# Performance work log

Hardware: AMD Instinct MI355X
Metric: run time of the kernel (lower is better)

The kernel has to match this reference:

```python
import jax, jax.numpy as jnp
import numpy as np

TARGET_MAIN_CONTRIBUTION = 0.6
CONTRIB_LOSS_COEF = 0.01
TOP_K = 2
NEG_INF = -1e9


def _gat(x, adj, W1, a1s, a1d, W2, a2s, a2d):
    """Dense 2-layer GAT (pyGAT style): multi-head concat + ELU, then one output head.
    x: [B,S,Fin], adj: [B,S,S], W1: [H,Fin,Fh], a1s/a1d: [H,Fh], W2: [H*Fh,Fout], a2s/a2d: [Fout]."""
    mask = adj > 0  # [B,S,S]
    h = jnp.einsum('bsf,hfo->bhso', x, W1)                      # [B,H,S,Fh]
    es = jnp.einsum('bhso,ho->bhs', h, a1s)
    ed = jnp.einsum('bhso,ho->bhs', h, a1d)
    e = jax.nn.leaky_relu(es[:, :, :, None] + ed[:, :, None, :], 0.2)  # [B,H,S,S]
    att = jax.nn.softmax(jnp.where(mask[:, None], e, NEG_INF), axis=-1)
    h1 = jax.nn.elu(jnp.einsum('bhst,bhto->bhso', att, h))      # [B,H,S,Fh]
    B, H, S, Fh = h1.shape
    h1 = h1.transpose(0, 2, 1, 3).reshape(B, S, H * Fh)         # concat heads
    h2 = h1 @ W2                                                # [B,S,Fout]
    e2 = jax.nn.leaky_relu((h2 @ a2s)[:, :, None] + (h2 @ a2d)[:, None, :], 0.2)
    att2 = jax.nn.softmax(jnp.where(mask, e2, NEG_INF), axis=-1)
    return jnp.einsum('bst,bto->bso', att2, h2)


def setup_inputs() -> dict:
    B, S, D, H, Hd, E = 4, 1024, 256, 6, 64, 3
    key = jax.random.key(0)
    ks = jax.random.split(key, 20)
    feature = jax.random.normal(ks[0], (B, S, D), dtype=jnp.float32)
    # sparse-ish binary adjacency with self-loops
    adj = (jax.random.uniform(ks[1], (B, S, S)) < 0.05).astype(jnp.float32)
    adj = jnp.maximum(adj, jnp.eye(S, dtype=jnp.float32)[None])
    p = lambda k, shape: jax.random.normal(k, shape, dtype=jnp.float32) * 0.1
    return {
        'feature': feature, 'adj': adj,
        'main_W1': p(ks[2], (H, D, Hd)), 'main_a1s': p(ks[3], (H, Hd)), 'main_a1d': p(ks[4], (H, Hd)),
        'main_W2': p(ks[5], (H * Hd, D)), 'main_a2s': p(ks[6], (D,)), 'main_a2d': p(ks[7], (D,)),
        'dep_W1': p(ks[8], (E, H, D, Hd)), 'dep_a1s': p(ks[9], (E, H, Hd)), 'dep_a1d': p(ks[10], (E, H, Hd)),
        'dep_W2': p(ks[11], (E, H * Hd, D)), 'dep_a2s': p(ks[12], (E, D)), 'dep_a2d': p(ks[13], (E, D)),
        'router_W': p(ks[14], (D, E)),
        'blend_W': p(ks[15], (D, D)), 'blend_b': jnp.zeros((D,), dtype=jnp.float32),
        'doc_num': 4, 'sect_num': 32,
    }


def reference(feature, adj, main_W1, main_a1s, main_a1d, main_W2, main_a2s, main_a2d,
              dep_W1, dep_a1s, dep_a1d, dep_W2, dep_a2s, dep_a2d,
              router_W, blend_W, blend_b, doc_num, sect_num):
    B, S, D = feature.shape
    E = router_W.shape[1]
    # main expert on full graph
    main_output = _gat(feature, adj, main_W1, main_a1s, main_a1d, main_W2, main_a2s, main_a2d)
    # per-expert adjacency views (zero out columns by node type)
    col = jnp.arange(S)
    sent_cols = (col < S - sect_num - doc_num).astype(adj.dtype)
    sect_cols = ((col >= S - sect_num - doc_num) & (col < S - doc_num)).astype(adj.dtype)
    doc_cols = (col >= S - doc_num).astype(adj.dtype)
    adj_stack = jnp.stack([adj * sent_cols, adj * sect_cols, adj * doc_cols])  # [E,B,S,S]
    # fixed top-k router
    x_flat = feature.reshape(-1, D)
    gate_probs = jax.nn.softmax(x_flat @ router_W, axis=-1)      # [B*S,E]
    _, top_idx = jax.lax.top_k(gate_probs, TOP_K)                # [B*S,k]
    routing_mask = jax.nn.one_hot(top_idx, E, dtype=feature.dtype).sum(axis=-2)  # [B*S,E] binary
    routing_mask = routing_mask.reshape(B, S, E)
    mask_e = routing_mask.transpose(2, 0, 1)[..., None]          # [E,B,S,1]
    # deputy experts: masked input, masked output, accumulate
    x_e = feature[None] * mask_e                                 # [E,B,S,D]
    dep_out = jax.vmap(_gat)(x_e, adj_stack, dep_W1, dep_a1s, dep_a1d, dep_W2, dep_a2s, dep_a2d)
    deputy_output = (dep_out * mask_e).sum(axis=0)               # [B,S,D]
    # blend gate
    blend_weight = jax.nn.sigmoid(feature @ blend_W + blend_b)
    final_output = blend_weight * main_output + (1.0 - blend_weight) * deputy_output
    main_contribution = blend_weight.mean()
    contribution_loss = jnp.abs(main_contribution - TARGET_MAIN_CONTRIBUTION) * CONTRIB_LOSS_COEF
    return final_output, contribution_loss, main_contribution
```

## Files before the change

kernel.cpp:

```cpp
#include <hip/hip_runtime.h>
#include <math.h>

#define B 4
#define S 1024
#define D 256
#define H 6
#define HD 64
#define NE 3
#define HHD 384
#define ROWS (B*S)
#define MAXN 128

typedef __attribute__((ext_vector_type(8))) short bf8_t;
typedef __attribute__((ext_vector_type(4))) float f32x4;

__device__ __forceinline__ float leaky(float x){ return x > 0.f ? x : 0.2f*x; }

__device__ __forceinline__ unsigned short f2bf(float f){
    union { float f; unsigned int u; } v; v.f = f;
    unsigned int u = v.u;
    return (unsigned short)((u + 0x7FFFu + ((u >> 16) & 1u)) >> 16);
}
__device__ __forceinline__ float bf2f(unsigned short h){
    union { unsigned int u; float f; } v; v.u = ((unsigned int)h) << 16;
    return v.f;
}
__device__ __forceinline__ float blo(unsigned int u){
    union { unsigned int u; float f; } v; v.u = u << 16; return v.f;
}
__device__ __forceinline__ float bhi(unsigned int u){
    union { unsigned int u; float f; } v; v.u = u & 0xffff0000u; return v.f;
}
__device__ __forceinline__ float i2f(int t){
    union { int i; float f; } v; v.i = t; return v.f;
}
__device__ __forceinline__ int f2i(float f){
    union { float f; int i; } v; v.f = f; return v.i;
}

#define PB_CONV   1024
#define PB_NBR    1024
#define PB_W1     1536
#define PB_W2     1536
#define PB_BW      256
#define PB_ZERO    177
#define PB_ROUTER 1024
#define PB_TOTAL  (PB_CONV + PB_NBR + PB_W1 + PB_W2 + PB_BW + PB_ZERO + PB_ROUTER)
#define NZERO     45088

__global__ __launch_bounds__(256) void prep_misc_kernel(
        const float* __restrict__ feature, const float* __restrict__ adj,
        const float* __restrict__ main_W1, const float* __restrict__ dep_W1,
        const float* __restrict__ main_W2, const float* __restrict__ dep_W2,
        const float* __restrict__ blend_W, const float* __restrict__ router_W,
        const int* __restrict__ doc_p, const int* __restrict__ sect_p,
        unsigned short* __restrict__ featbf, short* __restrict__ nbr,
        int4* __restrict__ nbc, unsigned short* __restrict__ w1nk,
        unsigned short* __restrict__ w2nk, unsigned short* __restrict__ bwt,
        float* __restrict__ zbase, float* __restrict__ rmask)
{
    int blk = blockIdx.x, tid = threadIdx.x;
    if (blk < PB_CONV){
        int idx = blk*256 + tid;
        float4 v = ((const float4*)feature)[idx];
        ushort4 o;
        o.x = f2bf(v.x); o.y = f2bf(v.y); o.z = f2bf(v.z); o.w = f2bf(v.w);
        ((ushort4*)featbf)[idx] = o;
        return;
    }
    blk -= PB_CONV;
    if (blk < PB_NBR){
        int wave = tid >> 6, lane = tid & 63;
        int row = blk*4 + wave;
        int b1 = S - *sect_p - *doc_p;
        int b2 = S - *doc_p;
        const float* ar = adj + (size_t)row*S + lane*16;
        float a[16];
        #pragma unroll
        for (int q = 0; q < 4; q++){
            float4 v = ((const float4*)ar)[q];
            a[q*4+0] = v.x; a[q*4+1] = v.y; a[q*4+2] = v.z; a[q*4+3] = v.w;
        }
        int t0 = lane*16;
        int k = 0, c1 = 0, c2 = 0;
        #pragma unroll
        for (int i = 0; i < 16; i++){
            if (a[i] > 0.f){
                k++;
                int t = t0 + i;
                if (t < b1) c1++;
                if (t < b2) c2++;
            }
        }
        int inc = k;
        #pragma unroll
        for (int d = 1; d < 64; d <<= 1){
            int u = __shfl_up(inc, d);
            if (lane >= d) inc += u;
        }
        int off = inc - k;
        int total = __shfl(inc, 63);
        int o = row*MAXN + off;
        #pragma unroll
        for (int i = 0; i < 16; i++){
            if (a[i] > 0.f) nbr[o++] = (short)(t0 + i);
        }
        for (int d = 32; d; d >>= 1){
            c1 += __shfl_down(c1, d);
            c2 += __shfl_down(c2, d);
        }
        if (lane == 0) nbc[row] = make_int4(total, c1, c2, 0);
        return;
    }
    blk -= PB_NBR;
    if (blk < PB_W1){
        int e = blk / 384;
        int idx = (blk - e*384)*256 + tid;
        const float* src = (e == 0) ? main_W1 : dep_W1 + (size_t)(e-1)*H*D*HD;
        int n = idx >> 8, k = idx & 255;
        int h = n >> 6, o = n & 63;
        w1nk[(size_t)e*HHD*D + idx] = f2bf(src[(h*D + k)*HD + o]);
        return;
    }
    blk -= PB_W1;
    if (blk < PB_W2){
        int g = blk*256 + tid;
        int e = g / (D*HHD);
        int rem = g - e*(D*HHD);
        int n = rem / HHD, k = rem - n*HHD;
        const float* src = (e == 0) ? main_W2 : dep_W2 + (size_t)(e-1)*HHD*D;
        w2nk[g] = f2bf(src[k*D + n]);
        return;
    }
    blk -= PB_W2;
    if (blk < PB_BW){
        int col = blk, k = tid;
        bwt[col*D + k] = f2bf(blend_W[k*D + col]);
        return;
    }
    blk -= PB_BW;
    if (blk < PB_ZERO){
        int idx = blk*256 + tid;
        if (idx < NZERO) zbase[idx] = 0.f;
        return;
    }
    blk -= PB_ZERO;
    {
        int wave = tid >> 6, lane = tid & 63;
        int row = blk*4 + wave;
        float4 xv = ((const float4*)(feature + (size_t)row*D))[lane];
        int f = lane*4;
        float xa[4] = {xv.x, xv.y, xv.z, xv.w};
        float p0 = 0.f, p1 = 0.f, p2 = 0.f;
        #pragma unroll
        for (int j = 0; j < 4; j++){
            p0 += xa[j]*router_W[(f+j)*NE + 0];
            p1 += xa[j]*router_W[(f+j)*NE + 1];
            p2 += xa[j]*router_W[(f+j)*NE + 2];
        }
        for (int off = 32; off; off >>= 1){
            p0 += __shfl_down(p0, off);
            p1 += __shfl_down(p1, off);
            p2 += __shfl_down(p2, off);
        }
        if (lane == 0){
            float p[3] = {p0, p1, p2};
            int ex = 0;
            for (int e = 1; e < NE; e++) if (p[e] <= p[ex]) ex = e;
            for (int e = 0; e < NE; e++) rmask[e*ROWS + row] = (e == ex) ? 0.f : 1.f;
        }
    }
}

__global__ __launch_bounds__(256) void gemm1_kernel(const unsigned short* __restrict__ w1nk,
                                                    const unsigned short* __restrict__ featbf,
                                                    const float* __restrict__ rmask,
                                                    const float* __restrict__ main_a1s,
                                                    const float* __restrict__ main_a1d,
                                                    const float* __restrict__ dep_a1s,
                                                    const float* __restrict__ dep_a1d,
                                                    unsigned short* __restrict__ htn4,
                                                    float* __restrict__ es8,
                                                    float* __restrict__ ed8,
                                                    float* __restrict__ meanV1p){
    __shared__ float ep[2][64][17];
    int tid = threadIdx.x, wave = tid >> 6, lane = tid & 63;
    int quad = lane >> 4, l16 = lane & 15;
    int e = blockIdx.z;
    int m0 = blockIdx.x*64;
    int n0 = blockIdx.y*64;
    const unsigned short* arow = w1nk + (size_t)e*HHD*D + (size_t)(m0 + wave*16 + l16)*D + quad*8;
    const unsigned short* brow[4];
    bool zr[4];
    #pragma unroll
    for (int j = 0; j < 4; j++){
        int n = n0 + j*16 + l16;
        brow[j] = featbf + (size_t)n*D + quad*8;
        zr[j] = (e > 0) ? (rmask[(size_t)(e-1)*ROWS + n] == 0.f) : false;
    }
    f32x4 z4 = {0.f,0.f,0.f,0.f};
    f32x4 acc[4] = {z4, z4, z4, z4};
    bf8_t bz = {0,0,0,0,0,0,0,0};
    for (int k0 = 0; k0 < D; k0 += 32){
        bf8_t a = *(const bf8_t*)(arow + k0);
        #pragma unroll
        for (int j = 0; j < 4; j++){
            bf8_t bv = zr[j] ? bz : *(const bf8_t*)(brow[j] + k0);
            acc[j] = __builtin_amdgcn_mfma_f32_16x16x32_bf16(a, bv, acc[j], 0, 0, 0);
        }
    }
    int b = n0 >> 10;
    int mbase = m0 + wave*16 + quad*4;
    int obase = wave*16 + quad*4;
    #pragma unroll
    for (int j = 0; j < 4; j++){
        int row = n0 + j*16 + l16;
        ushort4 o;
        o.x = f2bf(acc[j][0]); o.y = f2bf(acc[j][1]);
        o.z = f2bf(acc[j][2]); o.w = f2bf(acc[j][3]);
        *(ushort4*)(htn4 + ((size_t)e*ROWS + row)*HHD + mbase) = o;
    }
    const float* a1sp = (e == 0) ? main_a1s : dep_a1s + (size_t)(e-1)*H*HD;
    const float* a1dp = (e == 0) ? main_a1d : dep_a1d + (size_t)(e-1)*H*HD;
    float a1sv[4], a1dv[4];
    #pragma unroll
    for (int r = 0; r < 4; r++){ a1sv[r] = a1sp[mbase + r]; a1dv[r] = a1dp[mbase + r]; }
    #pragma unroll
    for (int j = 0; j < 4; j++){
        float ps = 0.f, pd = 0.f;
        #pragma unroll
        for (int r = 0; r < 4; r++){ ps += acc[j][r]*a1sv[r]; pd += acc[j][r]*a1dv[r]; }
        ep[0][j*16 + l16][wave*4 + quad] = ps;
        ep[1][j*16 + l16][wave*4 + quad] = pd;
    }
    #pragma unroll
    for (int r = 0; r < 4; r++){
        float cm = acc[0][r] + acc[1][r] + acc[2][r] + acc[3][r];
        for (int off = 8; off; off >>= 1) cm += __shfl_down(cm, off, 16);
        if (l16 == 0)
            atomicAdd(meanV1p + ((size_t)e*B + b)*512 + (obase + r)*8 + blockIdx.x,
                      cm*(1.f/(float)S));
    }
    __syncthreads();
    if (tid < 128){
        int arr = tid >> 6, sl = tid & 63;
        float sum = 0.f;
        #pragma unroll
        for (int i = 0; i < 16; i++) sum += ep[arr][sl][i];
        int n = n0 + sl;
        float* dst = arr ? ed8 : es8;
        dst[(((size_t)e*B + (n >> 10))*S + (n & 1023))*8 + blockIdx.x] = sum;
    }
}

__global__ __launch_bounds__(256) void remap1_kernel(const unsigned short* __restrict__ htn4,
                                                     unsigned short* __restrict__ V1p,
                                                     const int* __restrict__ doc_p,
                                                     const int* __restrict__ sect_p){
    int t = blockIdx.x, b = blockIdx.y, e = blockIdx.z;
    int b1 = S - *sect_p - *doc_p;
    int b2 = S - *doc_p;
    if (e == 1 && t >= b1) return;
    if (e == 2 && (t < b1 || t >= b2)) return;
    if (e == 3 && t < b2) return;
    if (e >= 2 && t < 960) return;
    unsigned short* dst;
    if (e < 2) dst = V1p + ((size_t)(e*B + b)*S + t)*512;
    else       dst = V1p + ((size_t)(2*B)*S + ((size_t)((e-2)*B + b))*64 + (t - 960))*512;
    const unsigned short* src = htn4 + ((size_t)e*ROWS + b*S + t)*HHD;
    int tid = threadIdx.x;
    int c0 = tid*2;
    int o = c0 >> 3, h = c0 & 7;
    unsigned short v0 = (h < 6)   ? src[h*64 + o]       : (unsigned short)0;
    unsigned short v1 = (h+1 < 6) ? src[(h+1)*64 + o]   : (unsigned short)0;
    ushort2 ov; ov.x = v0; ov.y = v1;
    *(ushort2*)(dst + c0) = ov;
}

__global__ __launch_bounds__(256) void attn1_gather_kernel(const unsigned short* __restrict__ V1p,
                                                           const float* __restrict__ es8,
                                                           const float* __restrict__ ed8,
                                                           const short* __restrict__ nbr,
                                                           const int4* __restrict__ nbc,
                                                           const float* __restrict__ meanV1p,
                                                           unsigned short* __restrict__ h1c4){
    __shared__ float wrec[4][MAXN][8];
    int wave = threadIdx.x >> 6, lane = threadIdx.x & 63;
    int s = blockIdx.x*4 + wave;
    int e = blockIdx.y >> 2, b = blockIdx.y & 3;
    int row = b*S + s;
    int4 c = nbc[row];
    int lo = 0, hi = c.x;
    if (e == 1) hi = c.y;
    else if (e == 2){ lo = c.y; hi = c.z; }
    else if (e == 3){ lo = c.z; }
    int nn = hi - lo;
    const float* esp = es8 + (((size_t)e*B + b)*S + s)*8;
    f32x4 es_lo = *(const f32x4*)esp;
    f32x4 es_hi = *(const f32x4*)(esp + 4);
    float esv[6] = {es_lo[0], es_lo[1], es_lo[2], es_lo[3], es_hi[0], es_hi[1]};
    const float* edb = ed8 + (((size_t)e*B + b)*S)*8;
    const short* nl = nbr + (size_t)row*MAXN;
    float w0[6] = {0,0,0,0,0,0}, w1[6] = {0,0,0,0,0,0};
    int t0 = 0, t1 = 0;
    if (lane < nn){
        t0 = nl[lo + lane];
        const float* ep = edb + (size_t)t0*8;
        f32x4 d0 = *(const f32x4*)ep;
        f32x4 d1 = *(const f32x4*)(ep + 4);
        float edv[6] = {d0[0], d0[1], d0[2], d0[3], d1[0], d1[1]};
        #pragma unroll
        for (int h = 0; h < 6; h++) w0[h] = __expf(leaky(esv[h] + edv[h]));
    }
    if (64 + lane < nn){
        t1 = nl[lo + 64 + lane];
        const float* ep = edb + (size_t)t1*8;
        f32x4 d0 = *(const f32x4*)ep;
        f32x4 d1 = *(const f32x4*)(ep + 4);
        float edv[6] = {d0[0], d0[1], d0[2], d0[3], d1[0], d1[1]};
        #pragma unroll
        for (int h = 0; h < 6; h++) w1[h] = __expf(leaky(esv[h] + edv[h]));
    }
    float den[6];
    #pragma unroll
    for (int h = 0; h < 6; h++){
        float d = w0[h] + w1[h];
        for (int o2 = 32; o2; o2 >>= 1) d += __shfl_down(d, o2);
        den[h] = __shfl(d, 0);
    }
    if (lane < nn){
        f32x4 r0 = {w0[0], w0[1], w0[2], w0[3]};
        f32x4 r1 = {w0[4], w0[5], i2f(t0), 0.f};
        *(f32x4*)&wrec[wave][lane][0] = r0;
        *(f32x4*)&wrec[wave][lane][4] = r1;
    }
    if (64 + lane < nn){
        f32x4 r0 = {w1[0], w1[1], w1[2], w1[3]};
        f32x4 r1 = {w1[4], w1[5], i2f(t1), 0.f};
        *(f32x4*)&wrec[wave][64 + lane][0] = r0;
        *(f32x4*)&wrec[wave][64 + lane][4] = r1;
    }
    const unsigned short* Vb;
    int toff;
    if (e < 2){ Vb = V1p + ((size_t)(e*B + b)*S)*512; toff = 0; }
    else      { Vb = V1p + ((size_t)(2*B)*S + ((size_t)((e-2)*B + b))*64)*512; toff = 960; }
    float acc[6] = {0,0,0,0,0,0};
    #pragma unroll 4
    for (int j = 0; j < nn; j++){
        f32x4 r0 = *(const f32x4*)&wrec[wave][j][0];
        f32x4 r1 = *(const f32x4*)&wrec[wave][j][4];
        int t = f2i(r1[2]);
        const unsigned short* vp = Vb + (size_t)(t - toff)*512 + lane*8;
        uint4 dv = *(const uint4*)vp;
        acc[0] += r0[0]*blo(dv.x); acc[1] += r0[1]*bhi(dv.x);
        acc[2] += r0[2]*blo(dv.y); acc[3] += r0[3]*bhi(dv.y);
        acc[4] += r1[0]*blo(dv.z); acc[5] += r1[1]*bhi(dv.z);
    }
    unsigned short* outp = h1c4 + ((size_t)e*ROWS + row)*HHD;
    const float* mv = meanV1p + ((size_t)e*B + b)*512 + lane*8;
    #pragma unroll
    for (int h = 0; h < 6; h++){
        float v = (nn > 0) ? acc[h]/den[h] : mv[h];
        v = v > 0.f ? v : __expf(v) - 1.f;
        outp[h*64 + lane] = f2bf(v);
    }
}

__global__ __launch_bounds__(256) void gemm2_kernel(const unsigned short* __restrict__ w2nk,
                                                    const unsigned short* __restrict__ h1c4,
                                                    const float* __restrict__ main_a2s,
                                                    const float* __restrict__ main_a2d,
                                                    const float* __restrict__ dep_a2s,
                                                    const float* __restrict__ dep_a2d,
                                                    unsigned short* __restrict__ h2n4,
                                                    float* __restrict__ f2s4,
                                                    float* __restrict__ f2d4,
                                                    float* __restrict__ meanV2){
    __shared__ float ep[2][64][17];
    int tid = threadIdx.x, wave = tid >> 6, lane = tid & 63;
    int quad = lane >> 4, l16 = lane & 15;
    int e = blockIdx.z;
    int m0 = blockIdx.x*64;
    int n0 = blockIdx.y*64;
    const unsigned short* arow = w2nk + (size_t)e*D*HHD + (size_t)(m0 + wave*16 + l16)*HHD + quad*8;
    const unsigned short* brow[4];
    #pragma unroll
    for (int j = 0; j < 4; j++)
        brow[j] = h1c4 + (size_t)e*ROWS*HHD + (size_t)(n0 + j*16 + l16)*HHD + quad*8;
    f32x4 z4 = {0.f,0.f,0.f,0.f};
    f32x4 acc[4] = {z4, z4, z4, z4};
    for (int k0 = 0; k0 < HHD; k0 += 32){
        bf8_t a = *(const bf8_t*)(arow + k0);
        #pragma unroll
        for (int j = 0; j < 4; j++){
            bf8_t bv = *(const bf8_t*)(brow[j] + k0);
            acc[j] = __builtin_amdgcn_mfma_f32_16x16x32_bf16(a, bv, acc[j], 0, 0, 0);
        }
    }
    int b = n0 >> 10;
    int mbase = m0 + wave*16 + quad*4;
    #pragma unroll
    for (int j = 0; j < 4; j++){
        int row = n0 + j*16 + l16;
        ushort4 o;
        o.x = f2bf(acc[j][0]); o.y = f2bf(acc[j][1]);
        o.z = f2bf(acc[j][2]); o.w = f2bf(acc[j][3]);
        *(ushort4*)(h2n4 + ((size_t)e*ROWS + row)*D + mbase) = o;
    }
    const float* a2sp = (e == 0) ? main_a2s : dep_a2s + (size_t)(e-1)*D;
    const float* a2dp = (e == 0) ? main_a2d : dep_a2d + (size_t)(e-1)*D;
    float a2sv[4], a2dv[4];
    #pragma unroll
    for (int r = 0; r < 4; r++){ a2sv[r] = a2sp[mbase + r]; a2dv[r] = a2dp[mbase + r]; }
    #pragma unroll
    for (int j = 0; j < 4; j++){
        float ps = 0.f, pd = 0.f;
        #pragma unroll
        for (int r = 0; r < 4; r++){ ps += acc[j][r]*a2sv[r]; pd += acc[j][r]*a2dv[r]; }
        ep[0][j*16 + l16][wave*4 + quad] = ps;
        ep[1][j*16 + l16][wave*4 + quad] = pd;
    }
    #pragma unroll
    for (int r = 0; r < 4; r++){
        float cm = acc[0][r] + acc[1][r] + acc[2][r] + acc[3][r];
        for (int off = 8; off; off >>= 1) cm += __shfl_down(cm, off, 16);
        if (l16 == 0)
            atomicAdd(meanV2 + ((size_t)e*B + b)*D + mbase + r, cm*(1.f/(float)S));
    }
    __syncthreads();
    if (tid < 128){
        int arr = tid >> 6, sl = tid & 63;
        float sum = 0.f;
        #pragma unroll
        for (int i = 0; i < 16; i++) sum += ep[arr][sl][i];
        int n = n0 + sl;
        float* dst = arr ? f2d4 : f2s4;
        atomicAdd(dst + (size_t)e*ROWS + n, sum);
    }
}

__global__ __launch_bounds__(256) void attn2_gather_kernel(const unsigned short* __restrict__ h2n4,
                                                           const float* __restrict__ f2s4,
                                                           const float* __restrict__ f2d4,
                                                           const short* __restrict__ nbr,
                                                           const int4* __restrict__ nbc,
                                                           const float* __restrict__ meanV2,
                                                           float* __restrict__ mainO,
                                                           unsigned short* __restrict__ depO3){
    __shared__ float2 wrec[4][MAXN];
    int wave = threadIdx.x >> 6, lane = threadIdx.x & 63;
    int s = blockIdx.x*4 + wave;
    int e = blockIdx.y >> 2, b = blockIdx.y & 3;
    int row = b*S + s;
    int4 c = nbc[row];
    int lo = 0, hi = c.x;
    if (e == 1) hi = c.y;
    else if (e == 2){ lo = c.y; hi = c.z; }
    else if (e == 3){ lo = c.z; }
    int nn = hi - lo;
    float fs_r = f2s4[(size_t)e*ROWS + row];
    const float* fdp = f2d4 + (size_t)e*ROWS + b*S;
    const short* nl = nbr + (size_t)row*MAXN;
    float w0 = 0.f, w1 = 0.f;
    int t0 = 0, t1 = 0;
    if (lane < nn){ t0 = nl[lo + lane]; w0 = __expf(leaky(fs_r + fdp[t0])); }
    if (64 + lane < nn){ t1 = nl[lo + 64 + lane]; w1 = __expf(leaky(fs_r + fdp[t1])); }
    float den = w0 + w1;
    for (int o2 = 32; o2; o2 >>= 1) den += __shfl_down(den, o2);
    den = __shfl(den, 0);
    if (lane < nn){ float2 r; r.x = w0; r.y = i2f(t0); wrec[wave][lane] = r; }
    if (64 + lane < nn){ float2 r; r.x = w1; r.y = i2f(t1); wrec[wave][64 + lane] = r; }
    const unsigned short* V = h2n4 + ((size_t)e*ROWS + b*S)*D;
    float acc[4] = {0,0,0,0};
    #pragma unroll 4
    for (int j = 0; j < nn; j++){
        float2 r = wrec[wave][j];
        float w = r.x;
        int t = f2i(r.y);
        const unsigned short* vp = V + (size_t)t*D + lane*4;
        uint2 dv = *(const uint2*)vp;
        acc[0] += w*blo(dv.x); acc[1] += w*bhi(dv.x);
        acc[2] += w*blo(dv.y); acc[3] += w*bhi(dv.y);
    }
    float out[4];
    if (nn > 0){
        float inv = 1.f/den;
        #pragma unroll
        for (int q = 0; q < 4; q++) out[q] = acc[q]*inv;
    } else {
        const float* mv = meanV2 + ((size_t)e*B + b)*D + lane*4;
        #pragma unroll
        for (int q = 0; q < 4; q++) out[q] = mv[q];
    }
    if (e == 0){
        *(float4*)(mainO + (size_t)row*D + lane*4) = make_float4(out[0], out[1], out[2], out[3]);
    } else {
        ushort4 o;
        o.x = f2bf(out[0]); o.y = f2bf(out[1]); o.z = f2bf(out[2]); o.w = f2bf(out[3]);
        *(ushort4*)(depO3 + (size_t)(e-1)*ROWS*D + (size_t)row*D + lane*4) = o;
    }
}

#define BLEND_NBLK ((ROWS/64)*(D/64))
__global__ __launch_bounds__(256) void blend_mfma_kernel(const unsigned short* __restrict__ featbf,
                                                         const unsigned short* __restrict__ bwt,
                                                         const float* __restrict__ bb,
                                                         const float* __restrict__ mainO,
                                                         const unsigned short* __restrict__ depO3,
                                                         const float* __restrict__ rmask,
                                                         float* __restrict__ outp,
                                                         float* __restrict__ sumBuf,
                                                         unsigned int* __restrict__ doneCnt){
    __shared__ float red[256];
    int tid = threadIdx.x, wave = tid >> 6, lane = tid & 63;
    int quad = lane >> 4, l16 = lane & 15;
    int m0 = blockIdx.x*64, n0 = blockIdx.y*64;
    const unsigned short* arow = featbf + (size_t)(m0 + wave*16 + l16)*D + quad*8;
    const unsigned short* brow[4];
    #pragma unroll
    for (int j = 0; j < 4; j++)
        brow[j] = bwt + (size_t)(n0 + j*16 + l16)*D + quad*8;
    f32x4 z4 = {0.f,0.f,0.f,0.f};
    f32x4 acc[4] = {z4, z4, z4, z4};
    for (int k0 = 0; k0 < D; k0 += 32){
        bf8_t a = *(const bf8_t*)(arow + k0);
        #pragma unroll
        for (int j = 0; j < 4; j++){
            bf8_t bv = *(const bf8_t*)(brow[j] + k0);
            acc[j] = __builtin_amdgcn_mfma_f32_16x16x32_bf16(a, bv, acc[j], 0, 0, 0);
        }
    }
    float lsum = 0.f;
    int mbase = m0 + wave*16 + quad*4;
    float rm[4][3];
    #pragma unroll
    for (int r = 0; r < 4; r++)
        #pragma unroll
        for (int e0 = 0; e0 < 3; e0++)
            rm[r][e0] = rmask[(size_t)e0*ROWS + mbase + r];
    #pragma unroll
    for (int j = 0; j < 4; j++){
        int col = n0 + j*16 + l16;
        float bias = bb[col];
        #pragma unroll
        for (int r = 0; r < 4; r++){
            size_t idx = (size_t)(mbase + r)*D + col;
            float dep = 0.f;
            #pragma unroll
            for (int e0 = 0; e0 < 3; e0++)
                dep += rm[r][e0]*bf2f(depO3[(size_t)e0*ROWS*D + idx]);
            float bw = 1.f/(1.f + __expf(-(acc[j][r] + bias)));
            lsum += bw;
            outp[idx] = bw*mainO[idx] + (1.f - bw)*dep;
        }
    }
    red[tid] = lsum;
    __syncthreads();
    for (int sft = 128; sft; sft >>= 1){
        if (tid < sft) red[tid] += red[tid + sft];
        __syncthreads();
    }
    if (tid == 0){
        atomicAdd(sumBuf, red[0]);
        __threadfence();
        unsigned int old = atomicAdd(doneCnt, 1u);
        if (old == BLEND_NBLK - 1){
            float total = atomicAdd(sumBuf, 0.f);
            float mc = total / (float)(ROWS*D);
            outp[ROWS*D]     = fabsf(mc - 0.6f)*0.01f;
            outp[ROWS*D + 1] = mc;
        }
    }
}

extern "C" void kernel_launch(void* const* d_in, const int* in_sizes, int n_in,
                              void* d_out, int out_size, void* d_ws, size_t ws_size,
                              hipStream_t stream)
{
    const float* feature  = (const float*)d_in[0];
    const float* adj      = (const float*)d_in[1];
    const float* main_W1  = (const float*)d_in[2];
    const float* main_a1s = (const float*)d_in[3];
    const float* main_a1d = (const float*)d_in[4];
    const float* main_W2  = (const float*)d_in[5];
    const float* main_a2s = (const float*)d_in[6];
    const float* main_a2d = (const float*)d_in[7];
    const float* dep_W1   = (const float*)d_in[8];
    const float* dep_a1s  = (const float*)d_in[9];
    const float* dep_a1d  = (const float*)d_in[10];
    const float* dep_W2   = (const float*)d_in[11];
    const float* dep_a2s  = (const float*)d_in[12];
    const float* dep_a2d  = (const float*)d_in[13];
    const float* router_W = (const float*)d_in[14];
    const float* blend_W  = (const float*)d_in[15];
    const float* blend_b  = (const float*)d_in[16];
    const int*   doc_p    = (const int*)d_in[17];
    const int*   sect_p   = (const int*)d_in[18];

    char* ws = (char*)d_ws;
    size_t off = 0;
    unsigned short* featbf = (unsigned short*)(ws + off); off += (size_t)ROWS*D*2;
    short*          nbr    = (short*)(ws + off);          off += (size_t)ROWS*MAXN*2;
    int4*           nbc    = (int4*)(ws + off);           off += (size_t)ROWS*16;
    unsigned short* w1nk   = (unsigned short*)(ws + off); off += (size_t)4*HHD*D*2;
    unsigned short* w2nk   = (unsigned short*)(ws + off); off += (size_t)4*D*HHD*2;
    unsigned short* bwt    = (unsigned short*)(ws + off); off += (size_t)D*D*2;
    float* es8 = (float*)(ws + off); off += (size_t)4*B*S*8*4;
    float* ed8 = (float*)(ws + off); off += (size_t)4*B*S*8*4;
    unsigned short* htn4 = (unsigned short*)(ws + off);
    float* mainO = (float*)(ws + off);
    unsigned short* depO3 = (unsigned short*)(ws + off + (size_t)ROWS*D*4);
    off += (size_t)4*ROWS*HHD*2;
    unsigned short* V1p  = (unsigned short*)(ws + off);
    unsigned short* h2n4 = (unsigned short*)(ws + off);
    {
        size_t v1sz = ((size_t)2*B*S + (size_t)2*B*64)*512*2;
        size_t h2sz = (size_t)4*ROWS*D*2;
        off += (v1sz > h2sz) ? v1sz : h2sz;
    }
    unsigned short* h1c4 = (unsigned short*)(ws + off); off += (size_t)4*ROWS*HHD*2;
    float* f2s4    = (float*)(ws + off); off += (size_t)4*ROWS*4;
    float* f2d4    = (float*)(ws + off); off += (size_t)4*ROWS*4;
    float* meanV1p = (float*)(ws + off); off += (size_t)4*B*512*4;
    float* meanV2  = (float*)(ws + off); off += (size_t)4*B*D*4;
    float* sumBuf  = (float*)(ws + off); off += 128;
    unsigned int* doneCnt = (unsigned int*)(sumBuf + 4);
    float* rmask   = (float*)(ws + off); off += (size_t)NE*ROWS*4;
    float* outp    = (float*)d_out;

    prep_misc_kernel<<<PB_TOTAL, 256, 0, stream>>>(
        feature, adj, main_W1, dep_W1, main_W2, dep_W2, blend_W, router_W,
        doc_p, sect_p, featbf, nbr, nbc, w1nk, w2nk, bwt, f2s4, rmask);

    gemm1_kernel<<<dim3(H, ROWS/64, 4), 256, 0, stream>>>(w1nk, featbf, rmask,
        main_a1s, main_a1d, dep_a1s, dep_a1d, htn4, es8, ed8, meanV1p);
    remap1_kernel<<<dim3(S, B, 4), 256, 0, stream>>>(htn4, V1p, doc_p, sect_p);
    attn1_gather_kernel<<<dim3(S/4, 16), 256, 0, stream>>>(V1p, es8, ed8, nbr, nbc,
        meanV1p, h1c4);
    gemm2_kernel<<<dim3(D/64, ROWS/64, 4), 256, 0, stream>>>(w2nk, h1c4,
        main_a2s, main_a2d, dep_a2s, dep_a2d, h2n4, f2s4, f2d4, meanV2);
    attn2_gather_kernel<<<dim3(S/4, 16), 256, 0, stream>>>(h2n4, f2s4, f2d4, nbr, nbc,
        meanV2, mainO, depO3);

    blend_mfma_kernel<<<dim3(ROWS/64, D/64), 256, 0, stream>>>(featbf, bwt, blend_b,
        mainO, depO3, rmask, outp, sumBuf, doneCnt);
}
```

Measured before the change: 243.3 us.

## Fuse V1 remap into gemm1 epilogue, retile blend kernel, deepen gather unroll

The gemm1 epilogue now writes its bf16 results straight into the head-interleaved V1p layout, with the expert-specific row-range filtering applied there. This removes the separate remap1 kernel along with the htn4 intermediate round trip through memory. The blend kernel is retiled to 16-row blocks with one MFMA tile per wave, giving four times as many blocks. The neighbour loops in both attention gathers are unrolled by 8 instead of 4. The cost is that the fused stores are strided 2-byte scatters, and the smaller blend blocks each reload their slice of bwt.

```diff
diff --git a/kernel.cpp b/kernel.cpp
--- a/kernel.cpp
+++ b/kernel.cpp
@@ -179,7 +179,9 @@
                                                     const float* __restrict__ main_a1d,
                                                     const float* __restrict__ dep_a1s,
                                                     const float* __restrict__ dep_a1d,
-                                                    unsigned short* __restrict__ htn4,
+                                                    const int* __restrict__ doc_p,
+                                                    const int* __restrict__ sect_p,
+                                                    unsigned short* __restrict__ V1p,
                                                     float* __restrict__ es8,
                                                     float* __restrict__ ed8,
                                                     float* __restrict__ meanV1p){
@@ -212,13 +214,34 @@
     int b = n0 >> 10;
     int mbase = m0 + wave*16 + quad*4;
     int obase = wave*16 + quad*4;
-    #pragma unroll
-    for (int j = 0; j < 4; j++){
-        int row = n0 + j*16 + l16;
-        ushort4 o;
-        o.x = f2bf(acc[j][0]); o.y = f2bf(acc[j][1]);
-        o.z = f2bf(acc[j][2]); o.w = f2bf(acc[j][3]);
-        *(ushort4*)(htn4 + ((size_t)e*ROWS + row)*HHD + mbase) = o;
+    int hh = blockIdx.x;
+    int b1v = S - *sect_p - *doc_p;
+    int b2v = S - *doc_p;
+    int tbase = n0 & 1023;
+    if (e <= 1){
+        unsigned short* dstb = V1p + (((size_t)(e*B + b))*S + tbase)*512 + hh;
+        #pragma unroll
+        for (int j = 0; j < 4; j++){
+            int t_l = j*16 + l16;
+            bool ok = (e == 0) || (tbase + t_l < b1v);
+            if (ok){
+                #pragma unroll
+                for (int r = 0; r < 4; r++)
+                    dstb[(size_t)t_l*512 + (size_t)(obase + r)*8] = f2bf(acc[j][r]);
+            }
+        }
+    } else if (tbase == 960){
+        unsigned short* dstb = V1p + ((size_t)(2*B)*S + ((size_t)((e-2)*B + b))*64)*512 + hh;
+        #pragma unroll
+        for (int j = 0; j < 4; j++){
+            int t = tbase + j*16 + l16;
+            bool ok = (e == 2) ? (t >= b1v && t < b2v) : (t >= b2v);
+            if (ok){
+                #pragma unroll
+                for (int r = 0; r < 4; r++)
+                    dstb[(size_t)(t - 960)*512 + (size_t)(obase + r)*8] = f2bf(acc[j][r]);
+            }
+        }
     }
     const float* a1sp = (e == 0) ? main_a1s : dep_a1s + (size_t)(e-1)*H*HD;
     const float* a1dp = (e == 0) ? main_a1d : dep_a1d + (size_t)(e-1)*H*HD;
@@ -238,7 +261,7 @@
         float cm = acc[0][r] + acc[1][r] + acc[2][r] + acc[3][r];
         for (int off = 8; off; off >>= 1) cm += __shfl_down(cm, off, 16);
         if (l16 == 0)
-            atomicAdd(meanV1p + ((size_t)e*B + b)*512 + (obase + r)*8 + blockIdx.x,
+            atomicAdd(meanV1p + ((size_t)e*B + b)*512 + (obase + r)*8 + hh,
                       cm*(1.f/(float)S));
     }
     __syncthreads();
@@ -249,32 +272,8 @@
         for (int i = 0; i < 16; i++) sum += ep[arr][sl][i];
         int n = n0 + sl;
         float* dst = arr ? ed8 : es8;
-        dst[(((size_t)e*B + (n >> 10))*S + (n & 1023))*8 + blockIdx.x] = sum;
-    }
-}
-
-__global__ __launch_bounds__(256) void remap1_kernel(const unsigned short* __restrict__ htn4,
-                                                     unsigned short* __restrict__ V1p,
-                                                     const int* __restrict__ doc_p,
-                                                     const int* __restrict__ sect_p){
-    int t = blockIdx.x, b = blockIdx.y, e = blockIdx.z;
-    int b1 = S - *sect_p - *doc_p;
-    int b2 = S - *doc_p;
-    if (e == 1 && t >= b1) return;
-    if (e == 2 && (t < b1 || t >= b2)) return;
-    if (e == 3 && t < b2) return;
-    if (e >= 2 && t < 960) return;
-    unsigned short* dst;
-    if (e < 2) dst = V1p + ((size_t)(e*B + b)*S + t)*512;
-    else       dst = V1p + ((size_t)(2*B)*S + ((size_t)((e-2)*B + b))*64 + (t - 960))*512;
-    const unsigned short* src = htn4 + ((size_t)e*ROWS + b*S + t)*HHD;
-    int tid = threadIdx.x;
-    int c0 = tid*2;
-    int o = c0 >> 3, h = c0 & 7;
-    unsigned short v0 = (h < 6)   ? src[h*64 + o]       : (unsigned short)0;
-    unsigned short v1 = (h+1 < 6) ? src[(h+1)*64 + o]   : (unsigned short)0;
-    ushort2 ov; ov.x = v0; ov.y = v1;
-    *(ushort2*)(dst + c0) = ov;
+        dst[(((size_t)e*B + (n >> 10))*S + (n & 1023))*8 + hh] = sum;
+    }
 }
 
 __global__ __launch_bounds__(256) void attn1_gather_kernel(const unsigned short* __restrict__ V1p,
@@ -345,7 +344,7 @@
     if (e < 2){ Vb = V1p + ((size_t)(e*B + b)*S)*512; toff = 0; }
     else      { Vb = V1p + ((size_t)(2*B)*S + ((size_t)((e-2)*B + b))*64)*512; toff = 960; }
     float acc[6] = {0,0,0,0,0,0};
-    #pragma unroll 4
+    #pragma unroll 8
     for (int j = 0; j < nn; j++){
         f32x4 r0 = *(const f32x4*)&wrec[wave][j][0];
         f32x4 r1 = *(const f32x4*)&wrec[wave][j][4];
@@ -472,7 +471,7 @@
     if (64 + lane < nn){ float2 r; r.x = w1; r.y = i2f(t1); wrec[wave][64 + lane] = r; }
     const unsigned short* V = h2n4 + ((size_t)e*ROWS + b*S)*D;
     float acc[4] = {0,0,0,0};
-    #pragma unroll 4
+    #pragma unroll 8
     for (int j = 0; j < nn; j++){
         float2 r = wrec[wave][j];
         float w = r.x;
@@ -501,7 +500,7 @@
     }
 }
 
-#define BLEND_NBLK ((ROWS/64)*(D/64))
+#define BLEND_NBLK ((ROWS/16)*(D/64))
 __global__ __launch_bounds__(256) void blend_mfma_kernel(const unsigned short* __restrict__ featbf,
                                                          const unsigned short* __restrict__ bwt,
                                                          const float* __restrict__ bb,
@@ -514,45 +513,30 @@
     __shared__ float red[256];
     int tid = threadIdx.x, wave = tid >> 6, lane = tid & 63;
     int quad = lane >> 4, l16 = lane & 15;
-    int m0 = blockIdx.x*64, n0 = blockIdx.y*64;
-    const unsigned short* arow = featbf + (size_t)(m0 + wave*16 + l16)*D + quad*8;
-    const unsigned short* brow[4];
-    #pragma unroll
-    for (int j = 0; j < 4; j++)
-        brow[j] = bwt + (size_t)(n0 + j*16 + l16)*D + quad*8;
-    f32x4 z4 = {0.f,0.f,0.f,0.f};
-    f32x4 acc[4] = {z4, z4, z4, z4};
+    int m0 = blockIdx.x*16, n0 = blockIdx.y*64;
+    const unsigned short* arow = featbf + (size_t)(m0 + l16)*D + quad*8;
+    const unsigned short* brow = bwt + (size_t)(n0 + wave*16 + l16)*D + quad*8;
+    f32x4 acc = {0.f,0.f,0.f,0.f};
     for (int k0 = 0; k0 < D; k0 += 32){
         bf8_t a = *(const bf8_t*)(arow + k0);
-        #pragma unroll
-        for (int j = 0; j < 4; j++){
-            bf8_t bv = *(const bf8_t*)(brow[j] + k0);
-            acc[j] = __builtin_amdgcn_mfma_f32_16x16x32_bf16(a, bv, acc[j], 0, 0, 0);
-        }
-    }
+        bf8_t bv = *(const bf8_t*)(brow + k0);
+        acc = __builtin_amdgcn_mfma_f32_16x16x32_bf16(a, bv, acc, 0, 0, 0);
+    }
+    int col = n0 + wave*16 + l16;
+    float bias = bb[col];
+    int mbase = m0 + quad*4;
     float lsum = 0.f;
-    int mbase = m0 + wave*16 + quad*4;
-    float rm[4][3];
-    #pragma unroll
-    for (int r = 0; r < 4; r++)
+    #pragma unroll
+    for (int r = 0; r < 4; r++){
+        int row = mbase + r;
+        size_t idx = (size_t)row*D + col;
+        float dep = 0.f;
         #pragma unroll
         for (int e0 = 0; e0 < 3; e0++)
-            rm[r][e0] = rmask[(size_t)e0*ROWS + mbase + r];
-    #pragma unroll
-    for (int j = 0; j < 4; j++){
-        int col = n0 + j*16 + l16;
-        float bias = bb[col];
-        #pragma unroll
-        for (int r = 0; r < 4; r++){
-            size_t idx = (size_t)(mbase + r)*D + col;
-            float dep = 0.f;
-            #pragma unroll
-            for (int e0 = 0; e0 < 3; e0++)
-                dep += rm[r][e0]*bf2f(depO3[(size_t)e0*ROWS*D + idx]);
-            float bw = 1.f/(1.f + __expf(-(acc[j][r] + bias)));
-            lsum += bw;
-            outp[idx] = bw*mainO[idx] + (1.f - bw)*dep;
-        }
+            dep += rmask[(size_t)e0*ROWS + row]*bf2f(depO3[(size_t)e0*ROWS*D + idx]);
+        float bw = 1.f/(1.f + __expf(-(acc[r] + bias)));
+        lsum += bw;
+        outp[idx] = bw*mainO[idx] + (1.f - bw)*dep;
     }
     red[tid] = lsum;
     __syncthreads();
@@ -607,10 +591,9 @@
     unsigned short* bwt    = (unsigned short*)(ws + off); off += (size_t)D*D*2;
     float* es8 = (float*)(ws + off); off += (size_t)4*B*S*8*4;
     float* ed8 = (float*)(ws + off); off += (size_t)4*B*S*8*4;
-    unsigned short* htn4 = (unsigned short*)(ws + off);
     float* mainO = (float*)(ws + off);
     unsigned short* depO3 = (unsigned short*)(ws + off + (size_t)ROWS*D*4);
-    off += (size_t)4*ROWS*HHD*2;
+    off += (size_t)ROWS*D*4 + (size_t)NE*ROWS*D*2;
     unsigned short* V1p  = (unsigned short*)(ws + off);
     unsigned short* h2n4 = (unsigned short*)(ws + off);
     {
@@ -633,8 +616,7 @@
         doc_p, sect_p, featbf, nbr, nbc, w1nk, w2nk, bwt, f2s4, rmask);
 
     gemm1_kernel<<<dim3(H, ROWS/64, 4), 256, 0, stream>>>(w1nk, featbf, rmask,
-        main_a1s, main_a1d, dep_a1s, dep_a1d, htn4, es8, ed8, meanV1p);
-    remap1_kernel<<<dim3(S, B, 4), 256, 0, stream>>>(htn4, V1p, doc_p, sect_p);
+        main_a1s, main_a1d, dep_a1s, dep_a1d, doc_p, sect_p, V1p, es8, ed8, meanV1p);
     attn1_gather_kernel<<<dim3(S/4, 16), 256, 0, stream>>>(V1p, es8, ed8, nbr, nbc,
         meanV1p, h1c4);
     gemm2_kernel<<<dim3(D/64, ROWS/64, 4), 256, 0, stream>>>(w2nk, h1c4,
@@ -642,6 +624,6 @@
     attn2_gather_kernel<<<dim3(S/4, 16), 256, 0, stream>>>(h2n4, f2s4, f2d4, nbr, nbc,
         meanV2, mainO, depO3);
 
-    blend_mfma_kernel<<<dim3(ROWS/64, D/64), 256, 0, stream>>>(featbf, bwt, blend_b,
+    blend_mfma_kernel<<<dim3(ROWS/16, D/64), 256, 0, stream>>>(featbf, bwt, blend_b,
         mainO, depO3, rmask, outp, sumBuf, doneCnt);
 }
```

Result: slower. 277.9 us (+14.2%).

## Fuse blend epilogue into attn2 gather and move blend GEMM into gemm1 launch

Applied to the files above, without the earlier changes.

The blend gate GEMM and sigmoid now run as an extra z-slice of the gemm1 launch, writing gate values to a buffer and accumulating their sum. The attn2 gather is restructured so each block handles one row with the four experts as four waves, staging their outputs in shared memory and applying the routing-masked blend directly. This removes the separate blend kernel launch and the round-trip of main and deputy outputs through global memory. In exchange it adds a float gate buffer write/read, and the attn2 grid shape changes, which may affect load balance. The contribution loss is now read from sumBuf by one thread, relying on the gemm1 atomics having completed in an earlier launch.

```diff
diff --git a/kernel.cpp b/kernel.cpp
--- a/kernel.cpp
+++ b/kernel.cpp
@@ -179,16 +179,67 @@
                                                     const float* __restrict__ main_a1d,
                                                     const float* __restrict__ dep_a1s,
                                                     const float* __restrict__ dep_a1d,
+                                                    const unsigned short* __restrict__ bwt,
+                                                    const float* __restrict__ bb,
                                                     unsigned short* __restrict__ htn4,
                                                     float* __restrict__ es8,
                                                     float* __restrict__ ed8,
-                                                    float* __restrict__ meanV1p){
+                                                    float* __restrict__ meanV1p,
+                                                    float* __restrict__ gatebuf,
+                                                    float* __restrict__ sumBuf){
     __shared__ float ep[2][64][17];
     int tid = threadIdx.x, wave = tid >> 6, lane = tid & 63;
     int quad = lane >> 4, l16 = lane & 15;
     int e = blockIdx.z;
+    int n0 = blockIdx.y*64;
+
+    if (e == 4){
+        if (blockIdx.x >= 4) return;
+        int m0 = blockIdx.x*64;
+        const unsigned short* arow = bwt + (size_t)(m0 + wave*16 + l16)*D + quad*8;
+        const unsigned short* brow[4];
+        #pragma unroll
+        for (int j = 0; j < 4; j++)
+            brow[j] = featbf + (size_t)(n0 + j*16 + l16)*D + quad*8;
+        f32x4 z4 = {0.f,0.f,0.f,0.f};
+        f32x4 acc[4] = {z4, z4, z4, z4};
+        for (int k0 = 0; k0 < D; k0 += 32){
+            bf8_t a = *(const bf8_t*)(arow + k0);
+            #pragma unroll
+            for (int j = 0; j < 4; j++){
+                bf8_t bv = *(const bf8_t*)(brow[j] + k0);
+                acc[j] = __builtin_amdgcn_mfma_f32_16x16x32_bf16(a, bv, acc[j], 0, 0, 0);
+            }
+        }
+        int mbase = m0 + wave*16 + quad*4;
+        float bias[4];
+        #pragma unroll
+        for (int r = 0; r < 4; r++) bias[r] = bb[mbase + r];
+        float lsum = 0.f;
+        #pragma unroll
+        for (int j = 0; j < 4; j++){
+            int rown = n0 + j*16 + l16;
+            f32x4 st;
+            #pragma unroll
+            for (int r = 0; r < 4; r++){
+                float g = 1.f/(1.f + __expf(-(acc[j][r] + bias[r])));
+                lsum += g;
+                st[r] = g;
+            }
+            *(f32x4*)(gatebuf + (size_t)rown*D + mbase) = st;
+        }
+        float* redp = &ep[0][0][0];
+        redp[tid] = lsum;
+        __syncthreads();
+        for (int sft = 128; sft; sft >>= 1){
+            if (tid < sft) redp[tid] += redp[tid + sft];
+            __syncthreads();
+        }
+        if (tid == 0) atomicAdd(sumBuf, redp[0]);
+        return;
+    }
+
     int m0 = blockIdx.x*64;
-    int n0 = blockIdx.y*64;
     const unsigned short* arow = w1nk + (size_t)e*HHD*D + (size_t)(m0 + wave*16 + l16)*D + quad*8;
     const unsigned short* brow[4];
     bool zr[4];
@@ -439,18 +490,21 @@
     }
 }
 
-__global__ __launch_bounds__(256) void attn2_gather_kernel(const unsigned short* __restrict__ h2n4,
-                                                           const float* __restrict__ f2s4,
-                                                           const float* __restrict__ f2d4,
-                                                           const short* __restrict__ nbr,
-                                                           const int4* __restrict__ nbc,
-                                                           const float* __restrict__ meanV2,
-                                                           float* __restrict__ mainO,
-                                                           unsigned short* __restrict__ depO3){
+__global__ __launch_bounds__(256) void attn2_blend_kernel(const unsigned short* __restrict__ h2n4,
+                                                          const float* __restrict__ f2s4,
+                                                          const float* __restrict__ f2d4,
+                                                          const short* __restrict__ nbr,
+                                                          const int4* __restrict__ nbc,
+                                                          const float* __restrict__ meanV2,
+                                                          const float* __restrict__ gatebuf,
+                                                          const float* __restrict__ rmask,
+                                                          const float* __restrict__ sumBuf,
+                                                          float* __restrict__ outp){
     __shared__ float2 wrec[4][MAXN];
+    __shared__ float outs[4][256];
     int wave = threadIdx.x >> 6, lane = threadIdx.x & 63;
-    int s = blockIdx.x*4 + wave;
-    int e = blockIdx.y >> 2, b = blockIdx.y & 3;
+    int s = blockIdx.x, b = blockIdx.y;
+    int e = wave;
     int row = b*S + s;
     int4 c = nbc[row];
     int lo = 0, hi = c.x;
@@ -482,94 +536,25 @@
         acc[0] += w*blo(dv.x); acc[1] += w*bhi(dv.x);
         acc[2] += w*blo(dv.y); acc[3] += w*bhi(dv.y);
     }
-    float out[4];
     if (nn > 0){
         float inv = 1.f/den;
         #pragma unroll
-        for (int q = 0; q < 4; q++) out[q] = acc[q]*inv;
+        for (int q = 0; q < 4; q++) outs[e][lane*4 + q] = acc[q]*inv;
     } else {
         const float* mv = meanV2 + ((size_t)e*B + b)*D + lane*4;
         #pragma unroll
-        for (int q = 0; q < 4; q++) out[q] = mv[q];
-    }
-    if (e == 0){
-        *(float4*)(mainO + (size_t)row*D + lane*4) = make_float4(out[0], out[1], out[2], out[3]);
-    } else {
-        ushort4 o;
-        o.x = f2bf(out[0]); o.y = f2bf(out[1]); o.z = f2bf(out[2]); o.w = f2bf(out[3]);
-        *(ushort4*)(depO3 + (size_t)(e-1)*ROWS*D + (size_t)row*D + lane*4) = o;
-    }
-}
-
-#define BLEND_NBLK ((ROWS/64)*(D/64))
-__global__ __launch_bounds__(256) void blend_mfma_kernel(const unsigned short* __restrict__ featbf,
-                                                         const unsigned short* __restrict__ bwt,
-                                                         const float* __restrict__ bb,
-                                                         const float* __restrict__ mainO,
-                                                         const unsigned short* __restrict__ depO3,
-                                                         const float* __restrict__ rmask,
-                                                         float* __restrict__ outp,
-                                                         float* __restrict__ sumBuf,
-                                                         unsigned int* __restrict__ doneCnt){
-    __shared__ float red[256];
-    int tid = threadIdx.x, wave = tid >> 6, lane = tid & 63;
-    int quad = lane >> 4, l16 = lane & 15;
-    int m0 = blockIdx.x*64, n0 = blockIdx.y*64;
-    const unsigned short* arow = featbf + (size_t)(m0 + wave*16 + l16)*D + quad*8;
-    const unsigned short* brow[4];
-    #pragma unroll
-    for (int j = 0; j < 4; j++)
-        brow[j] = bwt + (size_t)(n0 + j*16 + l16)*D + quad*8;
-    f32x4 z4 = {0.f,0.f,0.f,0.f};
-    f32x4 acc[4] = {z4, z4, z4, z4};
-    for (int k0 = 0; k0 < D; k0 += 32){
-        bf8_t a = *(const bf8_t*)(arow + k0);
-        #pragma unroll
-        for (int j = 0; j < 4; j++){
-            bf8_t bv = *(const bf8_t*)(brow[j] + k0);
-            acc[j] = __builtin_amdgcn_mfma_f32_16x16x32_bf16(a, bv, acc[j], 0, 0, 0);
-        }
-    }
-    float lsum = 0.f;
-    int mbase = m0 + wave*16 + quad*4;
-    float rm[4][3];
-    #pragma unroll
-    for (int r = 0; r < 4; r++)
-        #pragma unroll
-        for (int e0 = 0; e0 < 3; e0++)
-            rm[r][e0] = rmask[(size_t)e0*ROWS + mbase + r];
-    #pragma unroll
-    for (int j = 0; j < 4; j++){
-        int col = n0 + j*16 + l16;
-        float bias = bb[col];
-        #pragma unroll
-        for (int r = 0; r < 4; r++){
-            size_t idx = (size_t)(mbase + r)*D + col;
-            float dep = 0.f;
-            #pragma unroll
-            for (int e0 = 0; e0 < 3; e0++)
-                dep += rm[r][e0]*bf2f(depO3[(size_t)e0*ROWS*D + idx]);
-            float bw = 1.f/(1.f + __expf(-(acc[j][r] + bias)));
-            lsum += bw;
-            outp[idx] = bw*mainO[idx] + (1.f - bw)*dep;
-        }
-    }
-    red[tid] = lsum;
+        for (int q = 0; q < 4; q++) outs[e][lane*4 + q] = mv[q];
+    }
     __syncthreads();
-    for (int sft = 128; sft; sft >>= 1){
-        if (tid < sft) red[tid] += red[tid + sft];
-        __syncthreads();
-    }
-    if (tid == 0){
-        atomicAdd(sumBuf, red[0]);
-        __threadfence();
-        unsigned int old = atomicAdd(doneCnt, 1u);
-        if (old == BLEND_NBLK - 1){
-            float total = atomicAdd(sumBuf, 0.f);
-            float mc = total / (float)(ROWS*D);
-            outp[ROWS*D]     = fabsf(mc - 0.6f)*0.01f;
-            outp[ROWS*D + 1] = mc;
-        }
+    int col = threadIdx.x;
+    float g = gatebuf[(size_t)row*D + col];
+    float rm0 = rmask[row], rm1 = rmask[ROWS + row], rm2 = rmask[2*ROWS + row];
+    float dep = rm0*outs[1][col] + rm1*outs[2][col] + rm2*outs[3][col];
+    outp[(size_t)row*D + col] = g*outs[0][col] + (1.f - g)*dep;
+    if (blockIdx.x == 0 && blockIdx.y == 0 && threadIdx.x == 0){
+        float mc = sumBuf[0] / (float)(ROWS*D);
+        outp[ROWS*D]     = fabsf(mc - 0.6f)*0.01f;
+        outp[ROWS*D + 1] = mc;
     }
 }
 
@@ -607,10 +592,8 @@
     unsigned short* bwt    = (unsigned short*)(ws + off); off += (size_t)D*D*2;
     float* es8 = (float*)(ws + off); off += (size_t)4*B*S*8*4;
     float* ed8 = (float*)(ws + off); off += (size_t)4*B*S*8*4;
-    unsigned short* htn4 = (unsigned short*)(ws + off);
-    float* mainO = (float*)(ws + off);
-    unsigned short* depO3 = (unsigned short*)(ws + off + (size_t)ROWS*D*4);
-    off += (size_t)4*ROWS*HHD*2;
+    float* gatebuf = (float*)(ws + off); off += (size_t)ROWS*D*4;
+    unsigned short* htn4 = (unsigned short*)(ws + off); off += (size_t)4*ROWS*HHD*2;
     unsigned short* V1p  = (unsigned short*)(ws + off);
     unsigned short* h2n4 = (unsigned short*)(ws + off);
     {
@@ -624,7 +607,6 @@
     float* meanV1p = (float*)(ws + off); off += (size_t)4*B*512*4;
     float* meanV2  = (float*)(ws + off); off += (size_t)4*B*D*4;
     float* sumBuf  = (float*)(ws + off); off += 128;
-    unsigned int* doneCnt = (unsigned int*)(sumBuf + 4);
     float* rmask   = (float*)(ws + off); off += (size_t)NE*ROWS*4;
     float* outp    = (float*)d_out;
 
@@ -632,16 +614,14 @@
         feature, adj, main_W1, dep_W1, main_W2, dep_W2, blend_W, router_W,
         doc_p, sect_p, featbf, nbr, nbc, w1nk, w2nk, bwt, f2s4, rmask);
 
-    gemm1_kernel<<<dim3(H, ROWS/64, 4), 256, 0, stream>>>(w1nk, featbf, rmask,
-        main_a1s, main_a1d, dep_a1s, dep_a1d, htn4, es8, ed8, meanV1p);
+    gemm1_kernel<<<dim3(H, ROWS/64, 5), 256, 0, stream>>>(w1nk, featbf, rmask,
+        main_a1s, main_a1d, dep_a1s, dep_a1d, bwt, blend_b,
+        htn4, es8, ed8, meanV1p, gatebuf, sumBuf);
     remap1_kernel<<<dim3(S, B, 4), 256, 0, stream>>>(htn4, V1p, doc_p, sect_p);
     attn1_gather_kernel<<<dim3(S/4, 16), 256, 0, stream>>>(V1p, es8, ed8, nbr, nbc,
         meanV1p, h1c4);
     gemm2_kernel<<<dim3(D/64, ROWS/64, 4), 256, 0, stream>>>(w2nk, h1c4,
         main_a2s, main_a2d, dep_a2s, dep_a2d, h2n4, f2s4, f2d4, meanV2);
-    attn2_gather_kernel<<<dim3(S/4, 16), 256, 0, stream>>>(h2n4, f2s4, f2d4, nbr, nbc,
-        meanV2, mainO, depO3);
-
-    blend_mfma_kernel<<<dim3(ROWS/64, D/64), 256, 0, stream>>>(featbf, bwt, blend_b,
-        mainO, depO3, rmask, outp, sumBuf, doneCnt);
-}
+    attn2_blend_kernel<<<dim3(S, B), 256, 0, stream>>>(h2n4, f2s4, f2d4, nbr, nbc,
+        meanV2, gatebuf, rmask, sumBuf, outp);
+}
```

Result: faster. 236.8 us (-2.6%).
